# Optimization experiments

Hardware: AMD Instinct MI355X
Metric: run time of the kernel (lower is better)

## Reference

```python
import jax, jax.numpy as jnp
import numpy as np

# Static diagonal offsets of the SparseDIA matrix (eqx static field).
OFFSETS = (-128, -64, -8, -1, 0, 1, 8, 64, 128)
N = 8192   # matrix dimension (diags.shape[1])
M = 4096   # number of dense columns in `other`


def setup_inputs() -> dict:
    key = jax.random.key(0)
    k1, k2 = jax.random.split(key)
    diags = jax.random.normal(k1, (len(OFFSETS), N), dtype=jnp.float32)
    other = jax.random.normal(k2, (N, M), dtype=jnp.float32)
    return {"diags": diags, "other": other}


def reference(diags, other):
    """SparseDIA._matmul_dense(left_matmul=True): out = A_dia @ other.

    For each static offset k, rows [top:bottom] of the output accumulate
    diag[start:end] (the valid part of the stored diagonal) times the
    matching rows of `other`. Offsets are Python ints, so all slices are
    static and jit-compatible.
    """
    n = other.shape[0]
    out = jnp.zeros_like(other)
    for k, offset in enumerate(OFFSETS):
        start = max(0, offset)
        end = min(n, n + offset)
        top = max(0, -offset)
        bottom = top + (end - start)
        out = out.at[top:bottom, :].add(
            diags[k, start:end, None] * other[start:end, :]
        )
    return out
```

## Files before the change

kernel.cpp:

```cpp
#include <hip/hip_runtime.h>


#define DIA_N 8192
#define DIA_M 4096
#define M4   (DIA_M / 4)
#define CB   8
#define BR   256
#define HALO 128
#define WIN  (BR + 2*HALO)
#define TR   8

typedef float f4 __attribute__((ext_vector_type(4)));

typedef __attribute__((address_space(3))) unsigned int       lds_uint;
typedef const __attribute__((address_space(1))) unsigned int glb_uint;

__global__ __launch_bounds__(256) void sparse_dia_kernel(
    const float* __restrict__ diags,
    const float* __restrict__ other,
    float* __restrict__ out)
{
    constexpr int OFF[9] = {-128, -64, -8, -1, 0, 1, 8, 64, 128};

    __shared__ f4    olds[WIN][CB];
    __shared__ float dlds[9 * BR];

    const int tid  = threadIdx.x;
    const int r0   = blockIdx.y * BR;
    const int cb4  = blockIdx.x * CB;

#pragma unroll
    for (int f = tid; f < 9 * BR; f += 256) {
        const int k = f >> 8;
        const int i = f & (BR - 1);
        const int q = r0 + i + OFF[k];
        dlds[f] = (q >= 0 && q < DIA_N) ? diags[k * DIA_N + q] : 0.f;
    }

    {
        const int wave = tid >> 6;
        const int lane = tid & 63;
        const int lrow = lane >> 3;
        const int lcol = lane & 7;
#pragma unroll
        for (int s = 0; s < 16; ++s) {
            const int chunk = wave * 16 + s;
            int q = r0 - HALO + chunk * 8 + lrow;
            q = (q < 0) ? 0 : (q >= DIA_N ? DIA_N - 1 : q);
            const float* src = other + ((size_t)q * DIA_M + (size_t)(cb4 + lcol) * 4);
            __builtin_amdgcn_global_load_lds(
                (glb_uint*)src,
                (lds_uint*)&olds[chunk * 8][0],
                16, 0, 0);
        }
    }

    __syncthreads();

    const int c  = tid & 7;
    const int rt = tid >> 3;

    const f4* __restrict__ ow = (const f4*)other; (void)ow;
    f4* __restrict__ out4 = (f4*)out;

#pragma unroll
    for (int j = 0; j < TR; ++j) {
        const int i  = rt * TR + j;
        const int rl = HALO + i;
        f4 a = (f4){0.f, 0.f, 0.f, 0.f};
#pragma unroll
        for (int k = 0; k < 9; ++k) {
            a += dlds[k * BR + i] * olds[rl + OFF[k]][c];
        }
        out4[(size_t)(r0 + i) * M4 + cb4 + c] = a;
    }
}

extern "C" void kernel_launch(void* const* d_in, const int* in_sizes, int n_in,
                              void* d_out, int out_size, void* d_ws, size_t ws_size,
                              hipStream_t stream) {
    const float* diags = (const float*)d_in[0];
    const float* other = (const float*)d_in[1];
    float* out         = (float*)d_out;

    dim3 block(256, 1, 1);
    dim3 grid(M4 / CB, DIA_N / BR, 1);
    sparse_dia_kernel<<<grid, block, 0, stream>>>(diags, other, out);
}
```

Before: 260.8 us.

## Stream row blocks through an LDS ring buffer with double-buffered prefetch

```diff
diff --git a/kernel.cpp b/kernel.cpp
--- a/kernel.cpp
+++ b/kernel.cpp
@@ -3,15 +3,15 @@
 
 #define DIA_N 8192
 #define DIA_M 4096
-#define M4   (DIA_M / 4)
-#define CB   8
-#define BR   256
-#define HALO 128
-#define WIN  (BR + 2*HALO)
-#define TR   8
+#define M4    (DIA_M / 4)
+#define CB    8
+#define BR    256
+#define HALO  128
+#define RING  768
+#define NB    16
+#define GROUP (BR * NB)
 
 typedef float f4 __attribute__((ext_vector_type(4)));
-
 typedef __attribute__((address_space(3))) unsigned int       lds_uint;
 typedef const __attribute__((address_space(1))) unsigned int glb_uint;
 
@@ -22,57 +22,94 @@
 {
     constexpr int OFF[9] = {-128, -64, -8, -1, 0, 1, 8, 64, 128};
 
-    __shared__ f4    olds[WIN][CB];
-    __shared__ float dlds[9 * BR];
+    __shared__ f4    ring[RING][CB];
+    __shared__ float dlds[2][9 * BR];
 
     const int tid  = threadIdx.x;
-    const int r0   = blockIdx.y * BR;
+    const int gr0  = blockIdx.y * GROUP;
     const int cb4  = blockIdx.x * CB;
 
-#pragma unroll
-    for (int f = tid; f < 9 * BR; f += 256) {
-        const int k = f >> 8;
-        const int i = f & (BR - 1);
-        const int q = r0 + i + OFF[k];
-        dlds[f] = (q >= 0 && q < DIA_N) ? diags[k * DIA_N + q] : 0.f;
-    }
+    const int wave = tid >> 6;
+    const int lane = tid & 63;
+    const int lrow = lane >> 3;
+    const int lcol = lane & 7;
 
-    {
-        const int wave = tid >> 6;
-        const int lane = tid & 63;
-        const int lrow = lane >> 3;
-        const int lcol = lane & 7;
+    auto stage_ring = [&](int slot0, int q0, int nrows) {
+        const int per_wave = (nrows / 8) / 4;
 #pragma unroll
         for (int s = 0; s < 16; ++s) {
-            const int chunk = wave * 16 + s;
-            int q = r0 - HALO + chunk * 8 + lrow;
+            if (s >= per_wave) break;
+            const int inst = wave * per_wave + s;
+            int q = q0 + inst * 8 + lrow;
             q = (q < 0) ? 0 : (q >= DIA_N ? DIA_N - 1 : q);
             const float* src = other + ((size_t)q * DIA_M + (size_t)(cb4 + lcol) * 4);
             __builtin_amdgcn_global_load_lds(
                 (glb_uint*)src,
-                (lds_uint*)&olds[chunk * 8][0],
+                (lds_uint*)&ring[slot0 + inst * 8][0],
                 16, 0, 0);
         }
-    }
+    };
 
+    auto stage_diag = [&](int buf, int t) {
+        const int bs = gr0 + t * BR;
+#pragma unroll
+        for (int k = 0; k < 9; ++k) {
+            const int q  = bs + tid + OFF[k];
+            const int qc = (q < 0) ? 0 : (q >= DIA_N ? DIA_N - 1 : q);
+            float v = diags[k * DIA_N + qc];
+            v = ((unsigned)q < (unsigned)DIA_N) ? v : 0.f;
+            dlds[buf][k * BR + tid] = v;
+        }
+    };
+
+    f4* __restrict__ out4 = (f4*)out;
+
+    stage_ring(0, gr0 - HALO, 2 * BR);
+    stage_diag(0, 0);
     __syncthreads();
 
     const int c  = tid & 7;
-    const int rt = tid >> 3;
+    const int i0 = (tid >> 3) * 8;
 
-    const f4* __restrict__ ow = (const f4*)other; (void)ow;
-    f4* __restrict__ out4 = (f4*)out;
+    for (int t = 0; t < NB; ++t) {
+        if (t + 1 < NB) {
+            const int u = 2 * BR + t * BR;
+            stage_ring(u % RING, gr0 - HALO + u, BR);
+            stage_diag((t + 1) & 1, t + 1);
+        }
+
+        const int buf  = t & 1;
+        const int base = (HALO + t * BR) % RING;
+        auto slot = [&](int x) { int s = base + x; return (s >= RING) ? s - RING : s; };
+
+        f4 vm = ring[slot(i0 - 1)][c];
+        f4 v0 = ring[slot(i0    )][c];
+        f4 vp = ring[slot(i0 + 1)][c];
 
 #pragma unroll
-    for (int j = 0; j < TR; ++j) {
-        const int i  = rt * TR + j;
-        const int rl = HALO + i;
-        f4 a = (f4){0.f, 0.f, 0.f, 0.f};
+        for (int j = 0; j < 8; ++j) {
+            const int i = i0 + j;
+            float dk[9];
 #pragma unroll
-        for (int k = 0; k < 9; ++k) {
-            a += dlds[k * BR + i] * olds[rl + OFF[k]][c];
+            for (int k = 0; k < 9; ++k) dk[k] = dlds[buf][k * BR + i];
+
+            f4 a = dk[4] * v0;
+            a += dk[3] * vm;
+            a += dk[5] * vp;
+            a += dk[2] * ring[slot(i - 8)][c];
+            a += dk[6] * ring[slot(i + 8)][c];
+            a += dk[0] * ring[slot(i - 128)][c];
+            a += dk[1] * ring[slot(i - 64)][c];
+            a += dk[7] * ring[slot(i + 64)][c];
+            a += dk[8] * ring[slot(i + 128)][c];
+
+            out4[(size_t)(gr0 + t * BR + i) * M4 + cb4 + c] = a;
+
+            vm = v0; v0 = vp;
+            if (j < 7) vp = ring[slot(i + 2)][c];
         }
-        out4[(size_t)(r0 + i) * M4 + cb4 + c] = a;
+
+        __syncthreads();
     }
 }
 
@@ -84,6 +121,6 @@
     float* out         = (float*)d_out;
 
     dim3 block(256, 1, 1);
-    dim3 grid(M4 / CB, DIA_N / BR, 1);
+    dim3 grid(M4 / CB, DIA_N / GROUP, 1);
     sparse_dia_kernel<<<grid, block, 0, stream>>>(diags, other, out);
 }
```

After: 251.0 us. 3.7% less time.
